# Performance work log

Measured on AMD Instinct MI355X. Metric: run time of the kernel, lower is better.

Reference implementation:

```python
import jax, jax.numpy as jnp
import numpy as np

NUM_ENVS = 16384
N = 12          # decision vars (4 legs x 3D force)
M_CON = 24      # 4 SOC cones (3 each) + 12-dim hardtanh box
A_MIN, A_MAX = -10.0, 10.0
ALPHA, BETA = 1.0, 1.0


def setup_inputs() -> dict:
    key = jax.random.key(0)
    k1, k2, k3, k4 = jax.random.split(key, 4)
    Mw = jax.random.normal(k1, (NUM_ENVS, N, N), dtype=jnp.float32) / np.sqrt(N)
    # P must be SPD for inv/solve as in the original QP setup
    P = Mw @ jnp.swapaxes(Mw, -1, -2) + jnp.eye(N, dtype=jnp.float32)
    q = jax.random.normal(k2, (NUM_ENVS, N), dtype=jnp.float32)
    H = jax.random.normal(k3, (NUM_ENVS, M_CON, N), dtype=jnp.float32) * 0.5
    b = jax.random.normal(k4, (NUM_ENVS, M_CON), dtype=jnp.float32)
    contact_filter = jnp.ones((NUM_ENVS, M_CON), dtype=jnp.float32)
    return {"P": P, "q": q, "H": H, "b": b, "contact_filter": contact_filter, "iters": 100}


def _project(z, cf):
    # z: [B, m, 1]. Faithful to torch: project_onto_soc's only in-place effect on z
    # is z_part *= (z_part[:, 2:3] > 0); the full cone projection result is
    # discarded (returned but never written back). Then hardtanh box, then contact filter.
    Bsz = z.shape[0]
    soc = z[:, :12].reshape(Bsz, 4, 3)               # 4 cones of dim 3
    soc = soc * (soc[:, :, 2:3] > 0)                 # zero cone block if z-component <= 0
    box = jnp.clip(z[:, 12:24], A_MIN, A_MAX)        # hardtanh
    z = jnp.concatenate([soc.reshape(Bsz, 12, 1), box], axis=1)
    return z * cf


def reference(P, q, H, b, contact_filter, iters):
    m = H.shape[1]
    q_ = q[..., None]                                # [B, n, 1]
    b_ = b[..., None]                                # [B, m, 1]
    cf = contact_filter[..., None]                   # [B, m, 1]
    Ht = jnp.swapaxes(H, -1, -2)
    I = jnp.eye(m, dtype=P.dtype)
    Fm = I - H @ jnp.linalg.inv(P + Ht @ H) @ Ht     # [B, m, m]
    mu = Fm @ (H @ jnp.linalg.solve(P, q_) - b_)     # [B, m, 1]
    A = jnp.concatenate([
        jnp.concatenate([Fm, BETA * Fm], axis=2),
        jnp.concatenate([ALPHA * (I - 2.0 * Fm), I - 2.0 * ALPHA * BETA * Fm], axis=2),
    ], axis=1)                                       # [B, 2m, 2m]
    Bv = jnp.concatenate([BETA * mu, -2.0 * ALPHA * BETA * mu], axis=1)  # [B, 2m, 1]

    def step(lz, _):
        lz = A @ lz + Bv
        lz = jnp.concatenate([lz[:, :m], _project(lz[:, m:], cf)], axis=1)
        return lz, None

    lz0 = jnp.zeros((P.shape[0], 2 * m, 1), dtype=P.dtype)
    lz, _ = jax.lax.scan(step, lz0, None, length=iters)
    x = jnp.linalg.pinv(H) @ (lz[:, m:] - b_)        # [B, n, 1]
    return x, lz
```

## Files before the change

kernel.cpp:

```cpp
#include <hip/hip_runtime.h>

#define EPB 32
#define BLOCK 256
#define HS 292
#define GS 148
#define SS 28

#define WFENCE() __builtin_amdgcn_wave_barrier()

#define DPP_XOR1 0xB1
#define DPP_XOR2 0x4E
#define DPP_HMIR 0x141

constexpr int GMAP[8] = {0, 1, 2, 3, 7, 6, 5, 4};

#define FMA4(acc, f, s)                                         \
  acc = fmaf((f).x, (s).x,                                      \
        fmaf((f).y, (s).y,                                      \
        fmaf((f).z, (s).z,                                      \
        fmaf((f).w, (s).w, (acc)))))

#define VFMA(acc, s, v)                                         \
  { (acc).x = fmaf((s), (v).x, (acc).x);                        \
    (acc).y = fmaf((s), (v).y, (acc).y);                        \
    (acc).z = fmaf((s), (v).z, (acc).z);                        \
    (acc).w = fmaf((s), (v).w, (acc).w); }

#define ADD4(A, B) { (A).x += (B).x; (A).y += (B).y; (A).z += (B).z; (A).w += (B).w; }

template<int CTRL>
__device__ __forceinline__ float dppv(float v) {
  return __int_as_float(__builtin_amdgcn_update_dpp(
      0, __float_as_int(v), CTRL, 0xF, 0xF, true));
}

template<int K>
__device__ __forceinline__ float getel(const float4& a, const float4& b, const float4& c) {
  if constexpr (K == 0) return a.x; else if constexpr (K == 1) return a.y;
  else if constexpr (K == 2) return a.z; else if constexpr (K == 3) return a.w;
  else if constexpr (K == 4) return b.x; else if constexpr (K == 5) return b.y;
  else if constexpr (K == 6) return b.z; else if constexpr (K == 7) return b.w;
  else if constexpr (K == 8) return c.x; else if constexpr (K == 9) return c.y;
  else if constexpr (K == 10) return c.z; else return c.w;
}
template<int K>
__device__ __forceinline__ void setel(float4& a, float4& b, float4& c, float v) {
  if constexpr (K == 0) a.x = v; else if constexpr (K == 1) a.y = v;
  else if constexpr (K == 2) a.z = v; else if constexpr (K == 3) a.w = v;
  else if constexpr (K == 4) b.x = v; else if constexpr (K == 5) b.y = v;
  else if constexpr (K == 6) b.z = v; else if constexpr (K == 7) b.w = v;
  else if constexpr (K == 8) c.x = v; else if constexpr (K == 9) c.y = v;
  else if constexpr (K == 10) c.z = v; else c.w = v;
}

template<int S>
__device__ __forceinline__ void putS(float4* m, float v) {
  constexpr int Q = S >> 2, R = S & 3;
  if constexpr (R == 0) m[Q].x = v;
  else if constexpr (R == 1) m[Q].y = v;
  else if constexpr (R == 2) m[Q].z = v;
  else m[Q].w = v;
}

__device__ __forceinline__ float dot12(float4 a0, float4 a1, float4 a2,
                                       const float* p) {
  const float4* p4 = (const float4*)p;
  float4 b0 = p4[0], b1 = p4[1], b2 = p4[2];
  float acc = 0.f;
  FMA4(acc, a0, b0); FMA4(acc, a1, b1); FMA4(acc, a2, b2);
  return acc;
}

template<int K>
__device__ __forceinline__ void pivot_pub(float4& a, float4& b, float4& c, float* piv) {
  float ip = 1.0f / getel<K>(a, b, c);
  setel<K>(a, b, c, 1.0f);
  a.x *= ip; a.y *= ip; a.z *= ip; a.w *= ip;
  b.x *= ip; b.y *= ip; b.z *= ip; b.w *= ip;
  c.x *= ip; c.y *= ip; c.z *= ip; c.w *= ip;
  float4* pv = (float4*)piv;
  pv[0] = a; pv[1] = b; pv[2] = c;
}

#define ELIM(f, A, B, C)                                              \
  { (A).x = fmaf(-(f), p0.x, (A).x); (A).y = fmaf(-(f), p0.y, (A).y); \
    (A).z = fmaf(-(f), p0.z, (A).z); (A).w = fmaf(-(f), p0.w, (A).w); \
    (B).x = fmaf(-(f), p1.x, (B).x); (B).y = fmaf(-(f), p1.y, (B).y); \
    (B).z = fmaf(-(f), p1.z, (B).z); (B).w = fmaf(-(f), p1.w, (B).w); \
    (C).x = fmaf(-(f), p2.x, (C).x); (C).y = fmaf(-(f), p2.y, (C).y); \
    (C).z = fmaf(-(f), p2.z, (C).z); (C).w = fmaf(-(f), p2.w, (C).w); }

template<int K>
__device__ __forceinline__ void rgj_step(float4& a0, float4& b0, float4& c0,
                                         float4& a1, float4& b1, float4& c1,
                                         float* piv, int t) {
  if constexpr (K < 8) {
    if (t == K) pivot_pub<K>(a0, b0, c0, piv);
  } else {
    if (t == K - 8) pivot_pub<K>(a1, b1, c1, piv);
  }
  WFENCE();
  const float4* pv = (const float4*)piv;
  float4 p0 = pv[0], p1 = pv[1], p2 = pv[2];
  {
    const bool own = (K < 8) && (t == K);
    float cur = getel<K>(a0, b0, c0);
    float f = own ? 0.0f : cur;
    setel<K>(a0, b0, c0, own ? cur : 0.0f);
    ELIM(f, a0, b0, c0);
  }
  {
    const bool own = (K >= 8) && (t == K - 8);
    float cur = getel<K>(a1, b1, c1);
    float f = own ? 0.0f : cur;
    setel<K>(a1, b1, c1, own ? cur : 0.0f);
    ELIM(f, a1, b1, c1);
  }
  WFENCE();
}

template<int K>
__device__ __forceinline__ void rgj_all(float4& a0, float4& b0, float4& c0,
                                        float4& a1, float4& b1, float4& c1,
                                        float* piv, int t) {
  rgj_step<K>(a0, b0, c0, a1, b1, c1, piv, t);
  if constexpr (K < 11) rgj_all<K + 1>(a0, b0, c0, a1, b1, c1, piv, t);
}

__device__ __forceinline__ void gram_rows(const float* myH, int t, int i1,
    float4& a0, float4& b0, float4& c0, float4& a1, float4& b1, float4& c1) {
  a0 = make_float4(0.f, 0.f, 0.f, 0.f);
  b0 = a0; c0 = a0; a1 = a0; b1 = a0; c1 = a0;
#pragma unroll
  for (int k = 0; k < 24; ++k) {
    const float4* hk = (const float4*)(myH + k * 12);
    float4 h0 = hk[0], h1 = hk[1], h2 = hk[2];
    float f0 = myH[k * 12 + t];
    float f1 = myH[k * 12 + i1];
    VFMA(a0, f0, h0); VFMA(b0, f0, h1); VFMA(c0, f0, h2);
    VFMA(a1, f1, h0); VFMA(b1, f1, h1); VFMA(c1, f1, h2);
  }
}

template<int g, int k>
__device__ __forceinline__ void slot3(const float* myH, int t,
    const float4* W0, const float4* W1, const float4* W2,
    float4* P0, float4* P1, float4* P2) {
  const int c = 3 * (t ^ GMAP[g]) + k;
  const float4* hc = (const float4*)(myH + c * 12);
  float4 h0 = hc[0], h1 = hc[1], h2 = hc[2];
  float d0 = 0.f, d1 = 0.f, d2 = 0.f;
  FMA4(d0, h0, W0[0]); FMA4(d0, h1, W0[1]); FMA4(d0, h2, W0[2]);
  FMA4(d1, h0, W1[0]); FMA4(d1, h1, W1[1]); FMA4(d1, h2, W1[2]);
  FMA4(d2, h0, W2[0]); FMA4(d2, h1, W2[1]); FMA4(d2, h2, W2[2]);
  constexpr int S = 3 * g + k;
  putS<S>(P0, ((g == 0 && k == 0) ? 1.0f : 0.0f) - d0);
  putS<S>(P1, ((g == 0 && k == 1) ? 1.0f : 0.0f) - d1);
  putS<S>(P2, ((g == 0 && k == 2) ? 1.0f : 0.0f) - d2);
}

template<int S>
__device__ __forceinline__ float bgat(const float* bB, int t) {
  constexpr int g = S / 3, k = S % 3;
  return bB[3 * (t ^ GMAP[g]) + k];
}

__global__ __attribute__((amdgpu_flat_work_group_size(BLOCK, BLOCK),
                          amdgpu_waves_per_eu(1, 4)))
void pdhg_kernel(const float* __restrict__ P, const float* __restrict__ q,
                 const float* __restrict__ H, const float* __restrict__ b,
                 const float* __restrict__ cf, const int* __restrict__ itp,
                 float* __restrict__ out, int Btot) {
  __shared__ __align__(16) float sH[EPB * HS];
  __shared__ __align__(16) float sGi[EPB * GS];
  __shared__ __align__(16) float sB[EPB * SS];
  __shared__ __align__(16) float sAux[EPB * SS];

  const int tid  = threadIdx.x;
  const int wq   = tid >> 6;
  const int lane = tid & 63;
  const int e    = wq * 8 + (lane >> 3);
  const int t    = lane & 7;
  const int env  = blockIdx.x * EPB + e;
  const int envW0 = blockIdx.x * EPB + wq * 8;
  const int niter = itp[0];
  const int r0w = 3 * t;
  const int i1 = (t < 4) ? t + 8 : t;

  {
    const float4* gH = (const float4*)(H + (size_t)envW0 * 288);
#pragma unroll
    for (int rep = 0; rep < 9; ++rep) {
      int i = lane + rep * 64;
      int ee = i / 72, off = i - ee * 72;
      *(float4*)&sH[(wq * 8 + ee) * HS + off * 4] = gH[i];
    }
    const float4* gP = (const float4*)(P + (size_t)envW0 * 144);
#pragma unroll
    for (int rep = 0; rep < 4; ++rep) {
      int i = lane + rep * 64;
      int ee = i / 36, off = i - ee * 36;
      *(float4*)&sGi[(wq * 8 + ee) * GS + off * 4] = gP[i];
    }
    { int i = lane + 256; if (lane < 32) {
        int ee = i / 36, off = i - ee * 36;
        *(float4*)&sGi[(wq * 8 + ee) * GS + off * 4] = gP[i]; } }
    const float4* gq = (const float4*)(q + (size_t)envW0 * 12);
    if (lane < 24) {
      int ee = lane / 3, off = lane - ee * 3;
      *(float4*)&sAux[(wq * 8 + ee) * SS + off * 4] = gq[lane];
    }
    const float4* gb = (const float4*)(b + (size_t)envW0 * 24);
    if (lane < 48) {
      int ee = lane / 6, off = lane - ee * 6;
      *(float4*)&sB[(wq * 8 + ee) * SS + off * 4] = gb[lane];
    }
  }
  WFENCE();

  const float* myH = &sH[e * HS];
  float* giB  = &sGi[e * GS];
  float* auxB = &sAux[e * SS];
  float* bBm  = &sB[e * SS];
  const float* bB = bBm;

  float4 g0a, g0b, g0c, g1a, g1b, g1c;
  gram_rows(myH, t, i1, g0a, g0b, g0c, g1a, g1b, g1c);
  {
    const float4* p0 = (const float4*)(giB + t * 12);
    const float4* p1 = (const float4*)(giB + i1 * 12);
    float4 q0 = p0[0], q1 = p0[1], q2 = p0[2];
    float4 r0 = p1[0], r1 = p1[1], r2 = p1[2];
    ADD4(g0a, q0); ADD4(g0b, q1); ADD4(g0c, q2);
    ADD4(g1a, r0); ADD4(g1b, r1); ADD4(g1c, r2);
  }
  rgj_all<0>(g0a, g0b, g0c, g1a, g1b, g1c, auxB + 12, t);

  {
    float4* w0 = (float4*)(giB + t * 12);
    w0[0] = g0a; w0[1] = g0b; w0[2] = g0c;
    if (t < 4) {
      float4* w1 = (float4*)(giB + (t + 8) * 12);
      w1[0] = g1a; w1[1] = g1b; w1[2] = g1c;
    }
  }
  float y0 = dot12(g0a, g0b, g0c, auxB);
  float y1 = dot12(g1a, g1b, g1c, auxB);
  WFENCE();
  auxB[12 + t] = y0;
  if (t < 4) auxB[20 + t] = y1;
  WFENCE();

  float4 hr0[3], hr1[3], hr2[3];
  { const float4* p = (const float4*)(myH + (r0w + 0) * 12); hr0[0]=p[0]; hr0[1]=p[1]; hr0[2]=p[2]; }
  { const float4* p = (const float4*)(myH + (r0w + 1) * 12); hr1[0]=p[0]; hr1[1]=p[1]; hr1[2]=p[2]; }
  { const float4* p = (const float4*)(myH + (r0w + 2) * 12); hr2[0]=p[0]; hr2[1]=p[1]; hr2[2]=p[2]; }
  float u0, u1, u2;
  {
    const float4* y4 = (const float4*)(auxB + 12);
    float4 ya = y4[0], yb = y4[1], yc = y4[2];
    u0 = 0.f; FMA4(u0, hr0[0], ya); FMA4(u0, hr0[1], yb); FMA4(u0, hr0[2], yc);
    u1 = 0.f; FMA4(u1, hr1[0], ya); FMA4(u1, hr1[1], yb); FMA4(u1, hr1[2], yc);
    u2 = 0.f; FMA4(u2, hr2[0], ya); FMA4(u2, hr2[1], yb); FMA4(u2, hr2[2], yc);
  }

  float4 W0[3], W1[3], W2[3];
  W0[0] = make_float4(0.f,0.f,0.f,0.f); W0[1] = W0[0]; W0[2] = W0[0];
  W1[0] = W0[0]; W1[1] = W0[0]; W1[2] = W0[0];
  W2[0] = W0[0]; W2[1] = W0[0]; W2[2] = W0[0];
#define ACC_W(c, EX)                                                   \
  { const float4* g4 = (const float4*)(giB + (c) * 12);                \
    float4 r0 = g4[0], r1 = g4[1], r2 = g4[2];                         \
    float k0 = hr0[(c) >> 2].EX, k1 = hr1[(c) >> 2].EX, k2 = hr2[(c) >> 2].EX; \
    VFMA(W0[0], k0, r0); VFMA(W0[1], k0, r1); VFMA(W0[2], k0, r2);     \
    VFMA(W1[0], k1, r0); VFMA(W1[1], k1, r1); VFMA(W1[2], k1, r2);     \
    VFMA(W2[0], k2, r0); VFMA(W2[1], k2, r1); VFMA(W2[2], k2, r2); }
  ACC_W(0, x) ACC_W(1, y) ACC_W(2,  z) ACC_W(3,  w)
  ACC_W(4, x) ACC_W(5, y) ACC_W(6,  z) ACC_W(7,  w)
  ACC_W(8, x) ACC_W(9, y) ACC_W(10, z) ACC_W(11, w)
#undef ACC_W

  float4 Pm0[6], Pm1[6], Pm2[6];
#define SL(g, k) slot3<g, k>(myH, t, W0, W1, W2, Pm0, Pm1, Pm2);
  SL(0,0) SL(0,1) SL(0,2)  SL(1,0) SL(1,1) SL(1,2)
  SL(2,0) SL(2,1) SL(2,2)  SL(3,0) SL(3,1) SL(3,2)
  SL(4,0) SL(4,1) SL(4,2)  SL(5,0) SL(5,1) SL(5,2)
  SL(6,0) SL(6,1) SL(6,2)  SL(7,0) SL(7,1) SL(7,2)
#undef SL

  float mu0, mu1, mu2;
  {
    float4 bg0 = make_float4(bgat<0>(bB,t),  bgat<1>(bB,t),  bgat<2>(bB,t),  bgat<3>(bB,t));
    float4 bg1 = make_float4(bgat<4>(bB,t),  bgat<5>(bB,t),  bgat<6>(bB,t),  bgat<7>(bB,t));
    float4 bg2 = make_float4(bgat<8>(bB,t),  bgat<9>(bB,t),  bgat<10>(bB,t), bgat<11>(bB,t));
    float4 bg3 = make_float4(bgat<12>(bB,t), bgat<13>(bB,t), bgat<14>(bB,t), bgat<15>(bB,t));
    float4 bg4 = make_float4(bgat<16>(bB,t), bgat<17>(bB,t), bgat<18>(bB,t), bgat<19>(bB,t));
    float4 bg5 = make_float4(bgat<20>(bB,t), bgat<21>(bB,t), bgat<22>(bB,t), bgat<23>(bB,t));
    float d0 = 0.f, d1 = 0.f, d2 = 0.f;
    FMA4(d0, Pm0[0], bg0); FMA4(d1, Pm1[0], bg0); FMA4(d2, Pm2[0], bg0);
    FMA4(d0, Pm0[1], bg1); FMA4(d1, Pm1[1], bg1); FMA4(d2, Pm2[1], bg1);
    FMA4(d0, Pm0[2], bg2); FMA4(d1, Pm1[2], bg2); FMA4(d2, Pm2[2], bg2);
    FMA4(d0, Pm0[3], bg3); FMA4(d1, Pm1[3], bg3); FMA4(d2, Pm2[3], bg3);
    FMA4(d0, Pm0[4], bg4); FMA4(d1, Pm1[4], bg4); FMA4(d2, Pm2[4], bg4);
    FMA4(d0, Pm0[5], bg5); FMA4(d1, Pm1[5], bg5); FMA4(d2, Pm2[5], bg5);
    mu0 = u0 - d0;
    mu1 = u1 - d1;
    mu2 = u2 - d2;
  }
  float cfr0 = cf[(size_t)env * 24 + r0w];
  float cfr1 = cf[(size_t)env * 24 + r0w + 1];
  float cfr2 = cf[(size_t)env * 24 + r0w + 2];

  const float plo  = (t < 4) ? -3.0e38f : -10.0f;
  const float phi  = (t < 4) ?  3.0e38f :  10.0f;
  const float pthr = (t < 4) ? 0.0f     : -3.0e38f;
  float l0 = 0.f, l1 = 0.f, l2 = 0.f, z0 = 0.f, z1 = 0.f, z2 = 0.f;
  for (int it = 0; it < niter; ++it) {
    float s0 = l0 + z0, s1 = l1 + z1, s2 = l2 + z2;
    float g3  = dppv<DPP_XOR1>(s0), g4  = dppv<DPP_XOR1>(s1), g5  = dppv<DPP_XOR1>(s2);
    float g6  = dppv<DPP_XOR2>(s0), g7  = dppv<DPP_XOR2>(s1), g8  = dppv<DPP_XOR2>(s2);
    float g9  = dppv<DPP_XOR2>(g3), g10 = dppv<DPP_XOR2>(g4), g11 = dppv<DPP_XOR2>(g5);
    float g12 = dppv<DPP_HMIR>(s0), g13 = dppv<DPP_HMIR>(s1), g14 = dppv<DPP_HMIR>(s2);
    float g15 = dppv<DPP_HMIR>(g3), g16 = dppv<DPP_HMIR>(g4), g17 = dppv<DPP_HMIR>(g5);
    float g18 = dppv<DPP_HMIR>(g6), g19 = dppv<DPP_HMIR>(g7), g20 = dppv<DPP_HMIR>(g8);
    float g21 = dppv<DPP_HMIR>(g9), g22 = dppv<DPP_HMIR>(g10), g23 = dppv<DPP_HMIR>(g11);
    float4 v0 = make_float4(s0,  s1,  s2,  g3);
    float4 v1 = make_float4(g4,  g5,  g6,  g7);
    float4 v2 = make_float4(g8,  g9,  g10, g11);
    float4 v3 = make_float4(g12, g13, g14, g15);
    float4 v4 = make_float4(g16, g17, g18, g19);
    float4 v5 = make_float4(g20, g21, g22, g23);
    float a0 = mu0, a1 = mu1, a2 = mu2, b0 = 0.f, b1 = 0.f, b2 = 0.f;
    FMA4(a0, Pm0[0], v0); FMA4(a1, Pm1[0], v0); FMA4(a2, Pm2[0], v0);
    FMA4(a0, Pm0[1], v1); FMA4(a1, Pm1[1], v1); FMA4(a2, Pm2[1], v1);
    FMA4(a0, Pm0[2], v2); FMA4(a1, Pm1[2], v2); FMA4(a2, Pm2[2], v2);
    FMA4(b0, Pm0[3], v3); FMA4(b1, Pm1[3], v3); FMA4(b2, Pm2[3], v3);
    FMA4(b0, Pm0[4], v4); FMA4(b1, Pm1[4], v4); FMA4(b2, Pm2[4], v4);
    FMA4(b0, Pm0[5], v5); FMA4(b1, Pm1[5], v5); FMA4(b2, Pm2[5], v5);
    float w0 = a0 + b0, w1 = a1 + b1, w2 = a2 + b2;
    float zp0 = fmaf(-2.0f, w0, s0);
    float zp1 = fmaf(-2.0f, w1, s1);
    float zp2 = fmaf(-2.0f, w2, s2);
    l0 = w0; l1 = w1; l2 = w2;
    bool gt = zp2 > pthr;
    float e0 = gt ? cfr0 : 0.0f;
    float e1 = gt ? cfr1 : 0.0f;
    float e2 = gt ? cfr2 : 0.0f;
    z0 = __builtin_amdgcn_fmed3f(zp0, plo, phi) * e0;
    z1 = __builtin_amdgcn_fmed3f(zp1, plo, phi) * e1;
    z2 = __builtin_amdgcn_fmed3f(zp2, plo, phi) * e2;
  }

  float* xout  = out;
  float* lzout = out + (size_t)Btot * 12;
  lzout[(size_t)env * 48 + r0w]          = l0;
  lzout[(size_t)env * 48 + r0w + 1]      = l1;
  lzout[(size_t)env * 48 + r0w + 2]      = l2;
  lzout[(size_t)env * 48 + 24 + r0w]     = z0;
  lzout[(size_t)env * 48 + 24 + r0w + 1] = z1;
  lzout[(size_t)env * 48 + 24 + r0w + 2] = z2;

  float bo0 = bB[r0w];
  float bo1 = bB[r0w + 1];
  float bo2 = bB[r0w + 2];
  WFENCE();
  auxB[r0w]     = z0 - bo0;
  auxB[r0w + 1] = z1 - bo1;
  auxB[r0w + 2] = z2 - bo2;
  WFENCE();

  float rv0 = 0.f, rv8 = 0.f;
  {
    const float4* a4 = (const float4*)auxB;
    float4 au0 = a4[0], au1 = a4[1], au2 = a4[2], au3 = a4[3], au4 = a4[4], au5 = a4[5];
#define RVS(k, AV) { rv0 = fmaf(myH[(k) * 12 + t],  (AV), rv0);   \
                     rv8 = fmaf(myH[(k) * 12 + i1], (AV), rv8); }
    RVS(0,  au0.x) RVS(1,  au0.y) RVS(2,  au0.z) RVS(3,  au0.w)
    RVS(4,  au1.x) RVS(5,  au1.y) RVS(6,  au1.z) RVS(7,  au1.w)
    RVS(8,  au2.x) RVS(9,  au2.y) RVS(10, au2.z) RVS(11, au2.w)
    RVS(12, au3.x) RVS(13, au3.y) RVS(14, au3.z) RVS(15, au3.w)
    RVS(16, au4.x) RVS(17, au4.y) RVS(18, au4.z) RVS(19, au4.w)
    RVS(20, au5.x) RVS(21, au5.y) RVS(22, au5.z) RVS(23, au5.w)
#undef RVS
  }

  gram_rows(myH, t, i1, g0a, g0b, g0c, g1a, g1b, g1c);
  WFENCE();
  auxB[t] = rv0;
  if (t < 4) auxB[t + 8] = rv8;
  WFENCE();
  rgj_all<0>(g0a, g0b, g0c, g1a, g1b, g1c, bBm, t);

  xout[(size_t)env * 12 + t] = dot12(g0a, g0b, g0c, auxB);
  if (t < 4)
    xout[(size_t)env * 12 + t + 8] = dot12(g1a, g1b, g1c, auxB);
}

extern "C" void kernel_launch(void* const* d_in, const int* in_sizes, int n_in,
                              void* d_out, int out_size, void* d_ws, size_t ws_size,
                              hipStream_t stream) {
  const float* P  = (const float*)d_in[0];
  const float* q  = (const float*)d_in[1];
  const float* H  = (const float*)d_in[2];
  const float* b  = (const float*)d_in[3];
  const float* cf = (const float*)d_in[4];
  const int*   it = (const int*)d_in[5];
  float* out = (float*)d_out;
  const int B = in_sizes[1] / 12;
  const int grid = B / EPB;
  pdhg_kernel<<<grid, BLOCK, 0, stream>>>(P, q, H, b, cf, it, out, B);
}
```

Baseline: 144.9 us.

## Pack iteration matvec into v_pk_fma pairs and shorten DPP gather chain

The per-iteration 24x3 matvec now keeps rows 0 and 1 as float2 pairs and uses packed FMA, with row 2 left scalar. The DPP gather swaps the XOR2-of-XOR1 step for a single quad_perm reversal, so the shuffle chain is one level shallower and the ordering of neighbour slots changes. The projection clamp and mask now run in packed form, and the loop is unrolled by two. This aims to cut VALU instruction count and latency on the serial 100-iteration loop. The risks are the cost of packing or broadcasting scalars into pairs, and getting the permuted slot mapping right.

```diff
diff --git a/kernel.cpp b/kernel.cpp
--- a/kernel.cpp
+++ b/kernel.cpp
@@ -10,9 +10,16 @@
 
 #define DPP_XOR1 0xB1
 #define DPP_XOR2 0x4E
+#define DPP_QP3  0x1B
 #define DPP_HMIR 0x141
 
 constexpr int GMAP[8] = {0, 1, 2, 3, 7, 6, 5, 4};
+
+typedef float f2 __attribute__((ext_vector_type(2)));
+
+__device__ __forceinline__ f2 pkfma(f2 a, f2 b, f2 c) {
+  return __builtin_elementwise_fma(a, b, c);
+}
 
 #define FMA4(acc, f, s)                                         \
   acc = fmaf((f).x, (s).x,                                      \
@@ -51,15 +58,6 @@
   else if constexpr (K == 6) b.z = v; else if constexpr (K == 7) b.w = v;
   else if constexpr (K == 8) c.x = v; else if constexpr (K == 9) c.y = v;
   else if constexpr (K == 10) c.z = v; else c.w = v;
-}
-
-template<int S>
-__device__ __forceinline__ void putS(float4* m, float v) {
-  constexpr int Q = S >> 2, R = S & 3;
-  if constexpr (R == 0) m[Q].x = v;
-  else if constexpr (R == 1) m[Q].y = v;
-  else if constexpr (R == 2) m[Q].z = v;
-  else m[Q].w = v;
 }
 
 __device__ __forceinline__ float dot12(float4 a0, float4 a1, float4 a2,
@@ -145,7 +143,7 @@
 template<int g, int k>
 __device__ __forceinline__ void slot3(const float* myH, int t,
     const float4* W0, const float4* W1, const float4* W2,
-    float4* P0, float4* P1, float4* P2) {
+    f2* pm01, float* pm2s) {
   const int c = 3 * (t ^ GMAP[g]) + k;
   const float4* hc = (const float4*)(myH + c * 12);
   float4 h0 = hc[0], h1 = hc[1], h2 = hc[2];
@@ -154,9 +152,9 @@
   FMA4(d1, h0, W1[0]); FMA4(d1, h1, W1[1]); FMA4(d1, h2, W1[2]);
   FMA4(d2, h0, W2[0]); FMA4(d2, h1, W2[1]); FMA4(d2, h2, W2[2]);
   constexpr int S = 3 * g + k;
-  putS<S>(P0, ((g == 0 && k == 0) ? 1.0f : 0.0f) - d0);
-  putS<S>(P1, ((g == 0 && k == 1) ? 1.0f : 0.0f) - d1);
-  putS<S>(P2, ((g == 0 && k == 2) ? 1.0f : 0.0f) - d2);
+  pm01[S].x = ((g == 0 && k == 0) ? 1.0f : 0.0f) - d0;
+  pm01[S].y = ((g == 0 && k == 1) ? 1.0f : 0.0f) - d1;
+  pm2s[S]   = ((g == 0 && k == 2) ? 1.0f : 0.0f) - d2;
 }
 
 template<int S>
@@ -164,6 +162,15 @@
   constexpr int g = S / 3, k = S % 3;
   return bB[3 * (t ^ GMAP[g]) + k];
 }
+
+#define MPV0(S) pm01[S].x
+#define MPV1(S) pm01[S].y
+#define MPV2(S) pm2s[S]
+#define MUQ(d, PV, q, bg)                                             \
+  d = fmaf(PV(4*(q)), (bg).x,                                         \
+      fmaf(PV(4*(q)+1), (bg).y,                                       \
+      fmaf(PV(4*(q)+2), (bg).z,                                       \
+      fmaf(PV(4*(q)+3), (bg).w, d))));
 
 __global__ __attribute__((amdgpu_flat_work_group_size(BLOCK, BLOCK),
                           amdgpu_waves_per_eu(1, 4)))
@@ -280,15 +287,15 @@
   ACC_W(8, x) ACC_W(9, y) ACC_W(10, z) ACC_W(11, w)
 #undef ACC_W
 
-  float4 Pm0[6], Pm1[6], Pm2[6];
-#define SL(g, k) slot3<g, k>(myH, t, W0, W1, W2, Pm0, Pm1, Pm2);
+  f2 pm01[24]; float pm2s[24];
+#define SL(g, k) slot3<g, k>(myH, t, W0, W1, W2, pm01, pm2s);
   SL(0,0) SL(0,1) SL(0,2)  SL(1,0) SL(1,1) SL(1,2)
   SL(2,0) SL(2,1) SL(2,2)  SL(3,0) SL(3,1) SL(3,2)
   SL(4,0) SL(4,1) SL(4,2)  SL(5,0) SL(5,1) SL(5,2)
   SL(6,0) SL(6,1) SL(6,2)  SL(7,0) SL(7,1) SL(7,2)
 #undef SL
 
-  float mu0, mu1, mu2;
+  f2 mu01; float mu2s;
   {
     float4 bg0 = make_float4(bgat<0>(bB,t),  bgat<1>(bB,t),  bgat<2>(bB,t),  bgat<3>(bB,t));
     float4 bg1 = make_float4(bgat<4>(bB,t),  bgat<5>(bB,t),  bgat<6>(bB,t),  bgat<7>(bB,t));
@@ -297,76 +304,86 @@
     float4 bg4 = make_float4(bgat<16>(bB,t), bgat<17>(bB,t), bgat<18>(bB,t), bgat<19>(bB,t));
     float4 bg5 = make_float4(bgat<20>(bB,t), bgat<21>(bB,t), bgat<22>(bB,t), bgat<23>(bB,t));
     float d0 = 0.f, d1 = 0.f, d2 = 0.f;
-    FMA4(d0, Pm0[0], bg0); FMA4(d1, Pm1[0], bg0); FMA4(d2, Pm2[0], bg0);
-    FMA4(d0, Pm0[1], bg1); FMA4(d1, Pm1[1], bg1); FMA4(d2, Pm2[1], bg1);
-    FMA4(d0, Pm0[2], bg2); FMA4(d1, Pm1[2], bg2); FMA4(d2, Pm2[2], bg2);
-    FMA4(d0, Pm0[3], bg3); FMA4(d1, Pm1[3], bg3); FMA4(d2, Pm2[3], bg3);
-    FMA4(d0, Pm0[4], bg4); FMA4(d1, Pm1[4], bg4); FMA4(d2, Pm2[4], bg4);
-    FMA4(d0, Pm0[5], bg5); FMA4(d1, Pm1[5], bg5); FMA4(d2, Pm2[5], bg5);
-    mu0 = u0 - d0;
-    mu1 = u1 - d1;
-    mu2 = u2 - d2;
-  }
-  float cfr0 = cf[(size_t)env * 24 + r0w];
-  float cfr1 = cf[(size_t)env * 24 + r0w + 1];
-  float cfr2 = cf[(size_t)env * 24 + r0w + 2];
-
-  const float plo  = (t < 4) ? -3.0e38f : -10.0f;
+    MUQ(d0, MPV0, 0, bg0) MUQ(d1, MPV1, 0, bg0) MUQ(d2, MPV2, 0, bg0)
+    MUQ(d0, MPV0, 1, bg1) MUQ(d1, MPV1, 1, bg1) MUQ(d2, MPV2, 1, bg1)
+    MUQ(d0, MPV0, 2, bg2) MUQ(d1, MPV1, 2, bg2) MUQ(d2, MPV2, 2, bg2)
+    MUQ(d0, MPV0, 3, bg3) MUQ(d1, MPV1, 3, bg3) MUQ(d2, MPV2, 3, bg3)
+    MUQ(d0, MPV0, 4, bg4) MUQ(d1, MPV1, 4, bg4) MUQ(d2, MPV2, 4, bg4)
+    MUQ(d0, MPV0, 5, bg5) MUQ(d1, MPV1, 5, bg5) MUQ(d2, MPV2, 5, bg5)
+    mu01.x = u0 - d0;
+    mu01.y = u1 - d1;
+    mu2s   = u2 - d2;
+  }
+  f2 cf01; float cf2v;
+  cf01.x = cf[(size_t)env * 24 + r0w];
+  cf01.y = cf[(size_t)env * 24 + r0w + 1];
+  cf2v   = cf[(size_t)env * 24 + r0w + 2];
+
   const float phi  = (t < 4) ?  3.0e38f :  10.0f;
   const float pthr = (t < 4) ? 0.0f     : -3.0e38f;
-  float l0 = 0.f, l1 = 0.f, l2 = 0.f, z0 = 0.f, z1 = 0.f, z2 = 0.f;
+  const f2 lo01 = {-phi, -phi};
+  const f2 hi01 = { phi,  phi};
+  f2 l01 = {0.f, 0.f}, z01 = {0.f, 0.f};
+  float l2 = 0.f, z2 = 0.f;
+#pragma unroll 2
   for (int it = 0; it < niter; ++it) {
-    float s0 = l0 + z0, s1 = l1 + z1, s2 = l2 + z2;
-    float g3  = dppv<DPP_XOR1>(s0), g4  = dppv<DPP_XOR1>(s1), g5  = dppv<DPP_XOR1>(s2);
-    float g6  = dppv<DPP_XOR2>(s0), g7  = dppv<DPP_XOR2>(s1), g8  = dppv<DPP_XOR2>(s2);
-    float g9  = dppv<DPP_XOR2>(g3), g10 = dppv<DPP_XOR2>(g4), g11 = dppv<DPP_XOR2>(g5);
-    float g12 = dppv<DPP_HMIR>(s0), g13 = dppv<DPP_HMIR>(s1), g14 = dppv<DPP_HMIR>(s2);
-    float g15 = dppv<DPP_HMIR>(g3), g16 = dppv<DPP_HMIR>(g4), g17 = dppv<DPP_HMIR>(g5);
-    float g18 = dppv<DPP_HMIR>(g6), g19 = dppv<DPP_HMIR>(g7), g20 = dppv<DPP_HMIR>(g8);
-    float g21 = dppv<DPP_HMIR>(g9), g22 = dppv<DPP_HMIR>(g10), g23 = dppv<DPP_HMIR>(g11);
-    float4 v0 = make_float4(s0,  s1,  s2,  g3);
-    float4 v1 = make_float4(g4,  g5,  g6,  g7);
-    float4 v2 = make_float4(g8,  g9,  g10, g11);
-    float4 v3 = make_float4(g12, g13, g14, g15);
-    float4 v4 = make_float4(g16, g17, g18, g19);
-    float4 v5 = make_float4(g20, g21, g22, g23);
-    float a0 = mu0, a1 = mu1, a2 = mu2, b0 = 0.f, b1 = 0.f, b2 = 0.f;
-    FMA4(a0, Pm0[0], v0); FMA4(a1, Pm1[0], v0); FMA4(a2, Pm2[0], v0);
-    FMA4(a0, Pm0[1], v1); FMA4(a1, Pm1[1], v1); FMA4(a2, Pm2[1], v1);
-    FMA4(a0, Pm0[2], v2); FMA4(a1, Pm1[2], v2); FMA4(a2, Pm2[2], v2);
-    FMA4(b0, Pm0[3], v3); FMA4(b1, Pm1[3], v3); FMA4(b2, Pm2[3], v3);
-    FMA4(b0, Pm0[4], v4); FMA4(b1, Pm1[4], v4); FMA4(b2, Pm2[4], v4);
-    FMA4(b0, Pm0[5], v5); FMA4(b1, Pm1[5], v5); FMA4(b2, Pm2[5], v5);
-    float w0 = a0 + b0, w1 = a1 + b1, w2 = a2 + b2;
-    float zp0 = fmaf(-2.0f, w0, s0);
-    float zp1 = fmaf(-2.0f, w1, s1);
+    f2 s01 = l01 + z01;
+    float s2 = l2 + z2;
+    float s0 = s01.x, s1 = s01.y;
+    float x1a = dppv<DPP_XOR1>(s0), x1b = dppv<DPP_XOR1>(s1), x1c = dppv<DPP_XOR1>(s2);
+    float x2a = dppv<DPP_XOR2>(s0), x2b = dppv<DPP_XOR2>(s1), x2c = dppv<DPP_XOR2>(s2);
+    float q3a = dppv<DPP_QP3>(s0),  q3b = dppv<DPP_QP3>(s1),  q3c = dppv<DPP_QP3>(s2);
+    float h0a = dppv<DPP_HMIR>(s0), h0b = dppv<DPP_HMIR>(s1), h0c = dppv<DPP_HMIR>(s2);
+    float h1a = dppv<DPP_HMIR>(x1a), h1b = dppv<DPP_HMIR>(x1b), h1c = dppv<DPP_HMIR>(x1c);
+    float h2a = dppv<DPP_HMIR>(x2a), h2b = dppv<DPP_HMIR>(x2b), h2c = dppv<DPP_HMIR>(x2c);
+    float h3a = dppv<DPP_HMIR>(q3a), h3b = dppv<DPP_HMIR>(q3b), h3c = dppv<DPP_HMIR>(q3c);
+    f2 A01 = mu01, B01 = {0.f, 0.f};
+    float a2 = mu2s, b2 = 0.f;
+#define STEPA(S, m) { f2 mm = {(m), (m)};                              \
+      A01 = pkfma(pm01[S], mm, A01); a2 = fmaf(pm2s[S], (m), a2); }
+#define STEPB(S, m) { f2 mm = {(m), (m)};                              \
+      B01 = pkfma(pm01[S], mm, B01); b2 = fmaf(pm2s[S], (m), b2); }
+    STEPA(0, s0)   STEPA(1, s1)   STEPA(2, s2)
+    STEPA(3, x1a)  STEPA(4, x1b)  STEPA(5, x1c)
+    STEPA(6, x2a)  STEPA(7, x2b)  STEPA(8, x2c)
+    STEPA(9, q3a)  STEPA(10, q3b) STEPA(11, q3c)
+    STEPB(12, h0a) STEPB(13, h0b) STEPB(14, h0c)
+    STEPB(15, h1a) STEPB(16, h1b) STEPB(17, h1c)
+    STEPB(18, h2a) STEPB(19, h2b) STEPB(20, h2c)
+    STEPB(21, h3a) STEPB(22, h3b) STEPB(23, h3c)
+#undef STEPA
+#undef STEPB
+    f2 w01 = A01 + B01;
+    float w2 = a2 + b2;
+    f2 zp01 = pkfma((f2){-2.f, -2.f}, w01, s01);
     float zp2 = fmaf(-2.0f, w2, s2);
-    l0 = w0; l1 = w1; l2 = w2;
+    l01 = w01; l2 = w2;
+    f2 c01 = __builtin_elementwise_min(__builtin_elementwise_max(zp01, lo01), hi01);
+    float c2 = __builtin_amdgcn_fmed3f(zp2, -phi, phi);
     bool gt = zp2 > pthr;
-    float e0 = gt ? cfr0 : 0.0f;
-    float e1 = gt ? cfr1 : 0.0f;
-    float e2 = gt ? cfr2 : 0.0f;
-    z0 = __builtin_amdgcn_fmed3f(zp0, plo, phi) * e0;
-    z1 = __builtin_amdgcn_fmed3f(zp1, plo, phi) * e1;
-    z2 = __builtin_amdgcn_fmed3f(zp2, plo, phi) * e2;
+    f2 m01 = c01 * cf01;
+    float m2 = c2 * cf2v;
+    z01.x = gt ? m01.x : 0.0f;
+    z01.y = gt ? m01.y : 0.0f;
+    z2    = gt ? m2    : 0.0f;
   }
 
   float* xout  = out;
   float* lzout = out + (size_t)Btot * 12;
-  lzout[(size_t)env * 48 + r0w]          = l0;
-  lzout[(size_t)env * 48 + r0w + 1]      = l1;
+  lzout[(size_t)env * 48 + r0w]          = l01.x;
+  lzout[(size_t)env * 48 + r0w + 1]      = l01.y;
   lzout[(size_t)env * 48 + r0w + 2]      = l2;
-  lzout[(size_t)env * 48 + 24 + r0w]     = z0;
-  lzout[(size_t)env * 48 + 24 + r0w + 1] = z1;
+  lzout[(size_t)env * 48 + 24 + r0w]     = z01.x;
+  lzout[(size_t)env * 48 + 24 + r0w + 1] = z01.y;
   lzout[(size_t)env * 48 + 24 + r0w + 2] = z2;
 
   float bo0 = bB[r0w];
   float bo1 = bB[r0w + 1];
   float bo2 = bB[r0w + 2];
   WFENCE();
-  auxB[r0w]     = z0 - bo0;
-  auxB[r0w + 1] = z1 - bo1;
-  auxB[r0w + 2] = z2 - bo2;
+  auxB[r0w]     = z01.x - bo0;
+  auxB[r0w + 1] = z01.y - bo1;
+  auxB[r0w + 2] = z2    - bo2;
   WFENCE();
 
   float rv0 = 0.f, rv8 = 0.f;
```

After: 145.9 us. No clear change (+0.6%).
